# Optimization experiments

Hardware: AMD Instinct MI355X
Metric: run time of the kernel (lower is better)

Reference implementation:

```python
import jax, jax.numpy as jnp
import numpy as np

HIDDEN = 4096
N_HEADS = 32
N_KV_HEADS = 8
HEAD_DIM = HIDDEN // N_HEADS  # 128
GROUPS = N_HEADS // N_KV_HEADS  # 4
ATTN_MULT = 0.08838834764831845  # 1/sqrt(head_dim)
MAX_ATTN_VAL = 30.0
NEG_INF = -1e30


def setup_inputs() -> dict:
    key = jax.random.key(0)
    ks = jax.random.split(key, 5)
    B, S = 2, 2048
    hidden_states = jax.random.normal(ks[0], (B, S, HIDDEN), dtype=jnp.float32)
    scale = 1.0 / np.sqrt(HIDDEN)
    Wq = jax.random.normal(ks[1], (HIDDEN, N_HEADS * HEAD_DIM), dtype=jnp.float32) * scale
    Wk = jax.random.normal(ks[2], (HIDDEN, N_KV_HEADS * HEAD_DIM), dtype=jnp.float32) * scale
    Wv = jax.random.normal(ks[3], (HIDDEN, N_KV_HEADS * HEAD_DIM), dtype=jnp.float32) * scale
    Wo = jax.random.normal(ks[4], (N_HEADS * HEAD_DIM, HIDDEN), dtype=jnp.float32) * scale
    return {"hidden_states": hidden_states, "Wq": Wq, "Wk": Wk, "Wv": Wv, "Wo": Wo}


def reference(hidden_states, Wq, Wk, Wv, Wo):
    B, S, _ = hidden_states.shape
    # projections
    q = (hidden_states @ Wq).reshape(B, S, N_HEADS, HEAD_DIM).transpose(0, 2, 1, 3)      # bhsd
    k = (hidden_states @ Wk).reshape(B, S, N_KV_HEADS, HEAD_DIM).transpose(0, 2, 1, 3)   # bksd
    v = (hidden_states @ Wv).reshape(B, S, N_KV_HEADS, HEAD_DIM).transpose(0, 2, 1, 3)
    # GQA: expand kv heads to query heads
    k = jnp.repeat(k, GROUPS, axis=1)  # [B, N_HEADS, S, D]
    v = jnp.repeat(v, GROUPS, axis=1)
    # scaled scores with Grok-style tanh soft-cap
    scores = jnp.einsum('bhqd,bhkd->bhqk', q, k) * ATTN_MULT
    scores = MAX_ATTN_VAL * jnp.tanh(scores / MAX_ATTN_VAL)
    # causal mask
    causal = jnp.tril(jnp.ones((S, S), dtype=bool))
    scores = jnp.where(causal[None, None], scores, NEG_INF)
    probs = jax.nn.softmax(scores.astype(jnp.float32), axis=-1).astype(v.dtype)
    out = jnp.einsum('bhqk,bhkd->bhqd', probs, v)          # [B, H, S, D]
    out = out.transpose(0, 2, 1, 3).reshape(B, S, N_HEADS * HEAD_DIM)
    return out @ Wo
```

## Files before the change

### kernel.cpp

```cpp
#include <hip/hip_runtime.h>
#include <hip/hip_bf16.h>
#include <type_traits>
#include <utility>
#include <cmath>

#define HIDDEN 4096
#define NHEADS 32
#define NKV 8
#define HD 128
#define BB 2
#define SS 2048
#define NTOK (BB*SS)
#define ATTN_MULT 0.08838834764831845f

using bf16x8 = __attribute__((ext_vector_type(8))) short;
using f32x4  = __attribute__((ext_vector_type(4))) float;

using gas = __attribute__((address_space(1))) const void;
using las = __attribute__((address_space(3))) void;

__device__ __forceinline__ unsigned short f2bf(float f){
  unsigned int u = __builtin_bit_cast(unsigned int, f);
  u += 0x7fffu + ((u >> 16) & 1u);
  return (unsigned short)(u >> 16);
}
__device__ __forceinline__ unsigned int cvtpk(float lo, float hi){
  unsigned int r;
  asm("v_cvt_pk_bf16_f32 %0, %1, %2" : "=v"(r) : "v"(lo), "v"(hi));
  return r;
}
__device__ __forceinline__ float exp2_hw(float x){
  float r;
  asm("v_exp_f32 %0, %1" : "=v"(r) : "v"(x));
  return r;
}

#define LOG2E 1.4426950408889634f
#define C1L  (-5.3433149e-4f)
#define C2L  (2.3748069e-7f)
#define B30L (-43.280851227f)

__global__ void cvt_f32_bf16_k(const float* __restrict__ in, unsigned short* __restrict__ out, int n8){
  int i = blockIdx.x * blockDim.x + threadIdx.x;
  if (i >= n8) return;
  const float4* p = (const float4*)in + (size_t)i * 2;
  float4 a = p[0], b = p[1];
  bf16x8 o;
  o[0]=f2bf(a.x); o[1]=f2bf(a.y); o[2]=f2bf(a.z); o[3]=f2bf(a.w);
  o[4]=f2bf(b.x); o[5]=f2bf(b.y); o[6]=f2bf(b.z); o[7]=f2bf(b.w);
  ((bf16x8*)out)[i] = o;
}

__global__ void transpose_cvt_k(const float* __restrict__ W, unsigned short* __restrict__ WT, int K, int N){
  __shared__ float tile[32][33];
  int n0 = blockIdx.x * 32, k0 = blockIdx.y * 32;
  int tx = threadIdx.x, ty = threadIdx.y;
  #pragma unroll
  for (int i = 0; i < 4; ++i)
    tile[ty*4+i][tx] = W[(size_t)(k0 + ty*4 + i) * N + n0 + tx];
  __syncthreads();
  #pragma unroll
  for (int i = 0; i < 4; ++i)
    WT[(size_t)(n0 + ty*4 + i) * K + k0 + tx] = f2bf(tile[tx][ty*4+i]);
}

__global__ void transpose_v_k(const unsigned short* __restrict__ in, unsigned short* __restrict__ out){
  __shared__ unsigned short tile[32][33];
  int c0 = blockIdx.x * 32, r0 = blockIdx.y * 32;
  int tx = threadIdx.x, ty = threadIdx.y;
  #pragma unroll
  for (int i = 0; i < 4; ++i)
    tile[ty*4+i][tx] = in[(size_t)(r0 + ty*4 + i) * 2048 + 1024 + c0 + tx];
  __syncthreads();
  #pragma unroll
  for (int i = 0; i < 4; ++i){
    int c = c0 + ty*4 + i, r = r0 + tx;
    out[((size_t)((r >> 11) * 1024 + c)) * 2048 + (r & 2047)] = tile[tx][ty*4+i];
  }
}

template<typename OutT>
__global__ __launch_bounds__(256, 3)
void gemm_bt_k(const unsigned short* __restrict__ A,
               const unsigned short* __restrict__ BT,
               OutT* __restrict__ C, int M, int N, int K){
  __shared__ __align__(16) unsigned short As[128*32];
  __shared__ __align__(16) unsigned short Bs[128*32];
  const int m0 = blockIdx.y * 128, n0 = blockIdx.x * 128;
  const int tid = threadIdx.x, w = tid >> 6, lane = tid & 63;
  const int wr = w >> 1, wc = w & 1;
  const int lrow = lane & 15, lk = (lane >> 4) * 8;
  const int arow = lane >> 2, acol = (lane & 3) * 8;

  f32x4 acc[4][4] = {};

  for (int k0 = 0; k0 < K; k0 += 32){
    #pragma unroll
    for (int i = 0; i < 2; ++i){
      int chunk = w*2 + i;
      const unsigned short* ga = A  + (size_t)(m0 + chunk*16 + arow) * K + k0 + acol;
      const unsigned short* gb = BT + (size_t)(n0 + chunk*16 + arow) * K + k0 + acol;
      __builtin_amdgcn_global_load_lds((gas*)ga, (las*)(As + chunk*512), 16, 0, 0);
      __builtin_amdgcn_global_load_lds((gas*)gb, (las*)(Bs + chunk*512), 16, 0, 0);
    }
    __syncthreads();
    bf16x8 af[4], bfr[4];
    #pragma unroll
    for (int m = 0; m < 4; ++m) af[m]  = *(const bf16x8*)&As[(wr*64 + m*16 + lrow)*32 + lk];
    #pragma unroll
    for (int n = 0; n < 4; ++n) bfr[n] = *(const bf16x8*)&Bs[(wc*64 + n*16 + lrow)*32 + lk];
    #pragma unroll
    for (int m = 0; m < 4; ++m)
      #pragma unroll
      for (int n = 0; n < 4; ++n)
        acc[m][n] = __builtin_amdgcn_mfma_f32_16x16x32_bf16(af[m], bfr[n], acc[m][n], 0, 0, 0);
    __syncthreads();
  }

  const int crow = (lane >> 4) * 4, ccol = lane & 15;
  #pragma unroll
  for (int m = 0; m < 4; ++m)
    #pragma unroll
    for (int n = 0; n < 4; ++n){
      size_t base = (size_t)(m0 + wr*64 + m*16 + crow) * N + n0 + wc*64 + n*16 + ccol;
      #pragma unroll
      for (int r = 0; r < 4; ++r){
        float v = acc[m][n][r];
        if constexpr (std::is_same<OutT, unsigned short>::value) C[base + (size_t)r*N] = f2bf(v);
        else                                                     C[base + (size_t)r*N] = v;
      }
    }
}

#define GBAR() asm volatile("s_barrier" ::: "memory")

#define GEMM_PHASE(P, VMN, STAGE_STMT)                                          \
  {                                                                             \
    bf16x8 af[2][2];                                                            \
    _Pragma("unroll") for (int mi = 0; mi < 2; ++mi)                            \
    _Pragma("unroll") for (int kk = 0; kk < 2; ++kk){                           \
      int row = wm*128 + (P)*32 + mi*16 + lrow;                                 \
      int c8 = (kk*4 + lhi) ^ (row & 7);                                        \
      af[mi][kk] = *(const bf16x8*)&As[cur][row*64 + c8*8];                     \
    }                                                                           \
    if ((P) == 0){                                                              \
      _Pragma("unroll") for (int nf = 0; nf < 4; ++nf)                          \
      _Pragma("unroll") for (int kk = 0; kk < 2; ++kk){                         \
        int row = wn*64 + nf*16 + lrow;                                         \
        int c8 = (kk*4 + lhi) ^ (row & 7);                                      \
        bf[nf][kk] = *(const bf16x8*)&Bs[cur][row*64 + c8*8];                   \
      }                                                                         \
    }                                                                           \
    STAGE_STMT;                                                                 \
    asm volatile("s_waitcnt vmcnt(" #VMN ")");                                  \
    GBAR();                                                                     \
    __builtin_amdgcn_s_setprio(1);                                              \
    _Pragma("unroll") for (int mi = 0; mi < 2; ++mi)                            \
    _Pragma("unroll") for (int nf = 0; nf < 4; ++nf)                            \
    _Pragma("unroll") for (int kk = 0; kk < 2; ++kk)                            \
      acc[(P)*2+mi][nf] = __builtin_amdgcn_mfma_f32_16x16x32_bf16(              \
          af[mi][kk], bf[nf][kk], acc[(P)*2+mi][nf], 0, 0, 0);                  \
    __builtin_amdgcn_s_setprio(0);                                              \
  }

template<typename OutT>
__global__ __launch_bounds__(512, 2)
void gemm8_k(const unsigned short* __restrict__ A,
             const unsigned short* __restrict__ BT,
             OutT* __restrict__ C, int M, int N, int K, float scale){
  __shared__ __align__(16) unsigned short As[2][256*64];
  __shared__ __align__(16) unsigned short Bs[2][256*64];

  const int nbx = N >> 8;
  const int id = blockIdx.x + blockIdx.y * nbx;
  const int nwg = nbx * (M >> 8);
  const int swz = (id & 7) * (nwg >> 3) + (id >> 3);
  const int m0 = (swz / nbx) << 8, n0 = (swz % nbx) << 8;

  const int tid = threadIdx.x, w = tid >> 6, lane = tid & 63;
  const int wm = w >> 2, wn = w & 3;
  const int lrow = lane & 15, lhi = lane >> 4;
  const int l3 = lane >> 3, k8l = lane & 7;
  const int NT = K >> 6;

  f32x4 acc[8][4] = {};
  bf16x8 bf[4][2];

  auto stageB = [&](int t, int s, int half){
    #pragma unroll
    for (int j = 0; j < 2; ++j){
      int row0 = half*128 + j*64 + w*8;
      int row = row0 + l3;
      const unsigned short* g = BT + (size_t)(n0 + row) * K + t*64 + ((k8l ^ (row & 7)) << 3);
      __builtin_amdgcn_global_load_lds((gas*)g, (las*)(&Bs[s][0] + row0*64), 16, 0, 0);
    }
  };
  auto stageA = [&](int t, int s, int g2){
    #pragma unroll
    for (int j = 0; j < 2; ++j){
      int g = g2 + j;
      int row0 = ((w >= 4) ? 128 : 0) + g*32 + (w & 3)*8;
      int row = row0 + l3;
      const unsigned short* ga = A + (size_t)(m0 + row) * K + t*64 + ((k8l ^ (row & 7)) << 3);
      __builtin_amdgcn_global_load_lds((gas*)ga, (las*)(&As[s][0] + row0*64), 16, 0, 0);
    }
  };

  stageB(0, 0, 0); stageB(0, 0, 1); stageA(0, 0, 0); stageA(0, 0, 2);
  asm volatile("s_waitcnt vmcnt(3)");
  GBAR();

  for (int t = 0; t < NT - 1; ++t){
    const int cur = t & 1, nxt = cur ^ 1;
    GEMM_PHASE(0, 4, stageB(t+1, nxt, 0));
    GEMM_PHASE(1, 5, stageB(t+1, nxt, 1));
    GEMM_PHASE(2, 6, stageA(t+1, nxt, 0));
    GEMM_PHASE(3, 3, stageA(t+1, nxt, 2));
  }
  {
    const int cur = (NT - 1) & 1;
    GEMM_PHASE(0, 2, (void)0);
    GEMM_PHASE(1, 1, (void)0);
    GEMM_PHASE(2, 0, (void)0);
    GEMM_PHASE(3, 0, (void)0);
  }

  #pragma unroll
  for (int mf = 0; mf < 8; ++mf)
    #pragma unroll
    for (int nf = 0; nf < 4; ++nf){
      size_t base = (size_t)(m0 + wm*128 + mf*16 + lhi*4) * N + n0 + wn*64 + nf*16 + lrow;
      #pragma unroll
      for (int r = 0; r < 4; ++r){
        float v = acc[mf][nf][r] * scale;
        if constexpr (std::is_same<OutT, unsigned short>::value) C[base + (size_t)r*N] = f2bf(v);
        else                                                     C[base + (size_t)r*N] = v;
      }
    }
}

__global__ __launch_bounds__(512, 2)
void attn_k(const unsigned short* __restrict__ Q,
            const unsigned short* __restrict__ KVp,
            const unsigned short* __restrict__ VTp,
            unsigned short* __restrict__ ctx){
  __shared__ __align__(16) unsigned short Ks[2][64*128];
  __shared__ __align__(16) unsigned short Vt[2][128*64];
  __shared__ __align__(16) unsigned short Ps[8][1024];

  const int Wb = blockIdx.x;
  const int xcd = Wb & 7, sI = Wb >> 3;
  const int gsub = sI >> 4;
  const int inner = sI & 15;
  const int hsH = inner >> 2;
  const int fi = inner & 3;
  const int group = xcd*2 + gsub;
  const int b = group >> 3, kvh = group & 7;
  const int h = kvh*4 + hsH;

  const int tid = threadIdx.x, w = tid >> 6, lane = tid & 63;
  const int lrow = lane & 15, lhi = lane >> 4;
  const int xorv = (lrow & 3) << 4;

  const unsigned short* Kbh  = KVp + (size_t)b * SS * 2048 + kvh * HD;
  const unsigned short* VTbh = VTp + ((size_t)b * 1024 + kvh * HD) * SS;

  auto STAGE = [&](int db, int t){
    #pragma unroll
    for (int it = 0; it < 2; ++it){
      int cbase = it*512 + w*64;
      int c = cbase + lane;
      int kkv = c >> 4, kc = c & 15;
      const unsigned short* gk = Kbh + (size_t)(t*64 + kkv) * 2048 + ((kc ^ (kkv & 7)) << 3);
      __builtin_amdgcn_global_load_lds((gas*)gk, (las*)(&Ks[db][0] + cbase*8), 16, 0, 0);
      int vd = c >> 3, vc = c & 7;
      const unsigned short* gv = VTbh + (size_t)vd * SS + t*64 + ((vc ^ ((vd ^ (vd >> 3)) & 7)) << 3);
      __builtin_amdgcn_global_load_lds((gas*)gv, (las*)(&Vt[db][0] + cbase*8), 16, 0, 0);
    }
  };

  #pragma unroll 1
  for (int ph = 0; ph < 2; ++ph){
    const int strip = ph ? (7 - fi) : fi;
    const int qwb = strip*256 + w*32;
    const int nt = strip*4 + 4;

    bf16x8 qf[2][4];
    {
      const unsigned short* qb = Q + (size_t)(b*SS + qwb + lrow) * 4096 + h*HD + lhi*8;
      #pragma unroll
      for (int qg = 0; qg < 2; ++qg)
        #pragma unroll
        for (int ks = 0; ks < 4; ++ks)
          qf[qg][ks] = *(const bf16x8*)(qb + (size_t)qg*16*4096 + ks*32);
    }

    f32x4 o[8][2] = {};
    float psum[2] = {0.f, 0.f};

    STAGE(0, 0);
    __syncthreads();

    for (int t = 0; t < nt; ++t){
      const int db = t & 1;
      if (t + 1 < nt) STAGE(db ^ 1, t + 1);

      if (t*64 <= qwb + 31){
        const char* Kc = (const char*)&Ks[db][0];
        const char* Vc = (const char*)&Vt[db][0];
        char* Pw = (char*)&Ps[w][0];

        auto body = [&](auto DIAG){
          #pragma unroll
          for (int hh = 0; hh < 2; ++hh){
            f32x4 sacc[2][2];
            #pragma unroll
            for (int cc = 0; cc < 2; ++cc){
              const int row = (hh*2 + cc)*16 + lrow;
              bf16x8 kf[4];
              #pragma unroll
              for (int ks = 0; ks < 4; ++ks){
                int kbyte = (row*256 + (ks*32 + lhi*8)*2) ^ ((row & 7) << 4);
                kf[ks] = *(const bf16x8*)(Kc + kbyte);
              }
              f32x4 s0 = {0.f,0.f,0.f,0.f}, s1 = {0.f,0.f,0.f,0.f};
              __builtin_amdgcn_s_setprio(1);
              #pragma unroll
              for (int ks = 0; ks < 4; ++ks){
                s0 = __builtin_amdgcn_mfma_f32_16x16x32_bf16(kf[ks], qf[0][ks], s0, 0, 0, 0);
                s1 = __builtin_amdgcn_mfma_f32_16x16x32_bf16(kf[ks], qf[1][ks], s1, 0, 0, 0);
              }
              __builtin_amdgcn_s_setprio(0);
              sacc[0][cc] = s0; sacc[1][cc] = s1;
            }

            #pragma unroll
            for (int qg = 0; qg < 2; ++qg){
              const int qglob = qwb + qg*16 + lrow;
              #pragma unroll
              for (int cc = 0; cc < 2; ++cc){
                float pv[4];
                #pragma unroll
                for (int r = 0; r < 4; ++r){
                  float s = __builtin_amdgcn_fmed3f(sacc[qg][cc][r], -25.f, 25.f);
                  float s2 = s*s, s4 = s2*s2;
                  float wv = __builtin_fmaf(s2, C1L, LOG2E);
                  wv = __builtin_fmaf(s4, C2L, wv);
                  float p = exp2_hw(__builtin_fmaf(s, wv, B30L));
                  if constexpr (decltype(DIAG)::value){
                    int kvg = t*64 + (hh*2 + cc)*16 + lhi*4 + r;
                    p = (kvg <= qglob) ? p : 0.f;
                  }
                  psum[qg] += p;
                  pv[r] = p;
                }
                uint2 pk;
                pk.x = cvtpk(pv[0], pv[1]);
                pk.y = cvtpk(pv[2], pv[3]);
                *(uint2*)(Pw + qg*1024 + lrow*64 + ((cc*32 + lhi*8) ^ xorv)) = pk;
              }
            }

            bf16x8 pf0 = *(const bf16x8*)(Pw +        lrow*64 + ((lhi*16) ^ xorv));
            bf16x8 pf1 = *(const bf16x8*)(Pw + 1024 + lrow*64 + ((lhi*16) ^ xorv));
            __builtin_amdgcn_s_setprio(1);
            #pragma unroll
            for (int df = 0; df < 8; ++df){
              int d = df*16 + lrow;
              int vbyte = (d*128 + (hh*32 + lhi*8)*2) ^ (((d ^ (d >> 3)) & 7) << 4);
              bf16x8 vf = *(const bf16x8*)(Vc + vbyte);
              o[df][0] = __builtin_amdgcn_mfma_f32_16x16x32_bf16(vf, pf0, o[df][0], 0, 0, 0);
              o[df][1] = __builtin_amdgcn_mfma_f32_16x16x32_bf16(vf, pf1, o[df][1], 0, 0, 0);
            }
            __builtin_amdgcn_s_setprio(0);
          }
        };
        if (t == (qwb >> 6)) body(std::true_type{});
        else                 body(std::false_type{});
      }
      __syncthreads();
    }

    #pragma unroll
    for (int qg = 0; qg < 2; ++qg){
      float sum = psum[qg];
      sum += __shfl_xor(sum, 16);
      sum += __shfl_xor(sum, 32);
      float inv = 1.f / sum;
      unsigned short* base = ctx + (size_t)(b*SS + qwb + qg*16 + lrow) * 4096 + h*HD + lhi*4;
      #pragma unroll
      for (int df = 0; df < 8; ++df){
        uint2 pk;
        pk.x = cvtpk(o[df][qg][0] * inv, o[df][qg][1] * inv);
        pk.y = cvtpk(o[df][qg][2] * inv, o[df][qg][3] * inv);
        *(uint2*)(base + df*16) = pk;
      }
    }
    __syncthreads();
  }
}

#define O_HSB   ((size_t)0)
#define O_WQT   ((size_t)33554432)
#define O_WKT   ((size_t)67108864)
#define O_WVT   ((size_t)75497472)
#define O_WOT   ((size_t)83886080)
#define O_Q     ((size_t)117440512)
#define O_KV    ((size_t)150994944)
#define O_CTX   ((size_t)167772160)
#define WS_NEED ((size_t)201326592)

extern "C" void kernel_launch(void* const* d_in, const int* in_sizes, int n_in,
                              void* d_out, int out_size, void* d_ws, size_t ws_size,
                              hipStream_t stream){
  if (ws_size < WS_NEED) return;
  const float* hs = (const float*)d_in[0];
  const float* Wq = (const float*)d_in[1];
  const float* Wk = (const float*)d_in[2];
  const float* Wv = (const float*)d_in[3];
  const float* Wo = (const float*)d_in[4];
  char* ws = (char*)d_ws;
  unsigned short* hsb = (unsigned short*)(ws + O_HSB);
  unsigned short* WqT = (unsigned short*)(ws + O_WQT);
  unsigned short* WkT = (unsigned short*)(ws + O_WKT);
  unsigned short* WvT = (unsigned short*)(ws + O_WVT);
  unsigned short* WoT = (unsigned short*)(ws + O_WOT);
  unsigned short* Qb  = (unsigned short*)(ws + O_Q);
  unsigned short* KVb = (unsigned short*)(ws + O_KV);
  unsigned short* ctxb= (unsigned short*)(ws + O_CTX);
  unsigned short* VTb = (unsigned short*)(ws + O_WQT);

  cvt_f32_bf16_k<<<dim3((NTOK*HIDDEN/8)/256), dim3(256), 0, stream>>>(hs, hsb, NTOK*HIDDEN/8);
  transpose_cvt_k<<<dim3(128,128), dim3(32,8), 0, stream>>>(Wq, WqT, 4096, 4096);
  transpose_cvt_k<<<dim3(32,128),  dim3(32,8), 0, stream>>>(Wk, WkT, 4096, 1024);
  transpose_cvt_k<<<dim3(32,128),  dim3(32,8), 0, stream>>>(Wv, WvT, 4096, 1024);
  transpose_cvt_k<<<dim3(128,128), dim3(32,8), 0, stream>>>(Wo, WoT, 4096, 4096);
  gemm8_k<unsigned short><<<dim3(16,16), dim3(512), 0, stream>>>(hsb, WqT, Qb, 4096, 4096, 4096, ATTN_MULT);
  gemm_bt_k<unsigned short><<<dim3(16,32), dim3(256), 0, stream>>>(hsb, WkT, KVb, 4096, 2048, 4096);
  transpose_v_k<<<dim3(32,128), dim3(32,8), 0, stream>>>(KVb, VTb);
  attn_k<<<dim3(256), dim3(512), 0, stream>>>(Qb, KVb, VTb, ctxb);
  gemm8_k<float><<<dim3(16,16), dim3(512), 0, stream>>>(ctxb, WoT, (float*)d_out, 4096, 4096, 4096, 1.0f);
}
```

Baseline: 501.9 us.

## Restructure GEMM main loop to one barrier per K-tile with bulk prefetch

Replaces the four-phase interleaved schedule, which had a waitcnt and barrier per phase, with one loop iteration per K-tile. Each iteration issues all next-tile global-to-LDS loads up front, reads the B fragments and half of the A fragments, then runs the MFMAs while loading the remaining A fragments. It waits for all loads and syncs once at the end. This cuts barrier count and synchronisation overhead, at the cost of more register pressure from holding all A fragments, coarser overlap, and a full vmcnt(0) drain every tile.

```diff
diff --git a/kernel.cpp b/kernel.cpp
--- a/kernel.cpp
+++ b/kernel.cpp
@@ -134,35 +134,6 @@
 
 #define GBAR() asm volatile("s_barrier" ::: "memory")
 
-#define GEMM_PHASE(P, VMN, STAGE_STMT)                                          \
-  {                                                                             \
-    bf16x8 af[2][2];                                                            \
-    _Pragma("unroll") for (int mi = 0; mi < 2; ++mi)                            \
-    _Pragma("unroll") for (int kk = 0; kk < 2; ++kk){                           \
-      int row = wm*128 + (P)*32 + mi*16 + lrow;                                 \
-      int c8 = (kk*4 + lhi) ^ (row & 7);                                        \
-      af[mi][kk] = *(const bf16x8*)&As[cur][row*64 + c8*8];                     \
-    }                                                                           \
-    if ((P) == 0){                                                              \
-      _Pragma("unroll") for (int nf = 0; nf < 4; ++nf)                          \
-      _Pragma("unroll") for (int kk = 0; kk < 2; ++kk){                         \
-        int row = wn*64 + nf*16 + lrow;                                         \
-        int c8 = (kk*4 + lhi) ^ (row & 7);                                      \
-        bf[nf][kk] = *(const bf16x8*)&Bs[cur][row*64 + c8*8];                   \
-      }                                                                         \
-    }                                                                           \
-    STAGE_STMT;                                                                 \
-    asm volatile("s_waitcnt vmcnt(" #VMN ")");                                  \
-    GBAR();                                                                     \
-    __builtin_amdgcn_s_setprio(1);                                              \
-    _Pragma("unroll") for (int mi = 0; mi < 2; ++mi)                            \
-    _Pragma("unroll") for (int nf = 0; nf < 4; ++nf)                            \
-    _Pragma("unroll") for (int kk = 0; kk < 2; ++kk)                            \
-      acc[(P)*2+mi][nf] = __builtin_amdgcn_mfma_f32_16x16x32_bf16(              \
-          af[mi][kk], bf[nf][kk], acc[(P)*2+mi][nf], 0, 0, 0);                  \
-    __builtin_amdgcn_s_setprio(0);                                              \
-  }
-
 template<typename OutT>
 __global__ __launch_bounds__(512, 2)
 void gemm8_k(const unsigned short* __restrict__ A,
@@ -207,22 +178,63 @@
   };
 
   stageB(0, 0, 0); stageB(0, 0, 1); stageA(0, 0, 0); stageA(0, 0, 2);
-  asm volatile("s_waitcnt vmcnt(3)");
+  asm volatile("s_waitcnt vmcnt(0)");
   GBAR();
 
-  for (int t = 0; t < NT - 1; ++t){
+  #pragma unroll 1
+  for (int t = 0; t < NT; ++t){
     const int cur = t & 1, nxt = cur ^ 1;
-    GEMM_PHASE(0, 4, stageB(t+1, nxt, 0));
-    GEMM_PHASE(1, 5, stageB(t+1, nxt, 1));
-    GEMM_PHASE(2, 6, stageA(t+1, nxt, 0));
-    GEMM_PHASE(3, 3, stageA(t+1, nxt, 2));
-  }
-  {
-    const int cur = (NT - 1) & 1;
-    GEMM_PHASE(0, 2, (void)0);
-    GEMM_PHASE(1, 1, (void)0);
-    GEMM_PHASE(2, 0, (void)0);
-    GEMM_PHASE(3, 0, (void)0);
+    const bool pre = (t + 1 < NT);
+
+    if (pre){ stageB(t+1, nxt, 0); stageB(t+1, nxt, 1); stageA(t+1, nxt, 0); stageA(t+1, nxt, 2); }
+
+    #pragma unroll
+    for (int nf = 0; nf < 4; ++nf)
+      #pragma unroll
+      for (int kk = 0; kk < 2; ++kk){
+        int row = wn*64 + nf*16 + lrow;
+        int c8 = (kk*4 + lhi) ^ (row & 7);
+        bf[nf][kk] = *(const bf16x8*)&Bs[cur][row*64 + c8*8];
+      }
+    bf16x8 af[4][2][2];
+    #pragma unroll
+    for (int P = 0; P < 2; ++P)
+      #pragma unroll
+      for (int mi = 0; mi < 2; ++mi)
+        #pragma unroll
+        for (int kk = 0; kk < 2; ++kk){
+          int row = wm*128 + P*32 + mi*16 + lrow;
+          int c8 = (kk*4 + lhi) ^ (row & 7);
+          af[P][mi][kk] = *(const bf16x8*)&As[cur][row*64 + c8*8];
+        }
+
+    __builtin_amdgcn_s_setprio(1);
+    #pragma unroll
+    for (int P = 0; P < 4; ++P){
+      if (P < 2){
+        const int Q = P + 2;
+        #pragma unroll
+        for (int mi = 0; mi < 2; ++mi)
+          #pragma unroll
+          for (int kk = 0; kk < 2; ++kk){
+            int row = wm*128 + Q*32 + mi*16 + lrow;
+            int c8 = (kk*4 + lhi) ^ (row & 7);
+            af[Q][mi][kk] = *(const bf16x8*)&As[cur][row*64 + c8*8];
+          }
+      }
+      #pragma unroll
+      for (int mi = 0; mi < 2; ++mi)
+        #pragma unroll
+        for (int nf = 0; nf < 4; ++nf)
+          #pragma unroll
+          for (int kk = 0; kk < 2; ++kk)
+            acc[P*2+mi][nf] = __builtin_amdgcn_mfma_f32_16x16x32_bf16(
+                af[P][mi][kk], bf[nf][kk], acc[P*2+mi][nf], 0, 0, 0);
+    }
+    __builtin_amdgcn_s_setprio(0);
+
+    if (pre) asm volatile("s_waitcnt vmcnt(0)");
+    GBAR();
   }
 
   #pragma unroll
```

New measurement: 531.8 us. 6.0% more time.
